# Kernel optimization log

Hardware: AMD Instinct MI355X
Metric: run time of the kernel (lower is better)

The kernel has to match this reference:

```python
import jax, jax.numpy as jnp
import numpy as np

DIM = 768
NUM_HEADS = 12
HEAD_DIM = DIM // NUM_HEADS
SCALE = HEAD_DIM ** -0.5


def setup_inputs() -> dict:
    key = jax.random.key(0)
    k1, k2, k3, k4 = jax.random.split(key, 4)
    B, N = 4, 2048
    x = jax.random.normal(k1, (B, N, DIM), dtype=jnp.float32)
    # torch Linear(dim, 3*dim, bias=False): weight [3*dim, dim]
    w_qkv = jax.random.normal(k2, (3 * DIM, DIM), dtype=jnp.float32) * (DIM ** -0.5)
    # proj: Linear(dim, dim) with bias
    w_proj = jax.random.normal(k3, (DIM, DIM), dtype=jnp.float32) * (DIM ** -0.5)
    b_proj = jax.random.normal(k4, (DIM,), dtype=jnp.float32) * 0.01
    return {"x": x, "w_qkv": w_qkv, "w_proj": w_proj, "b_proj": b_proj}


def reference(x, w_qkv, w_proj, b_proj):
    B, N, D = x.shape
    H, Hd = NUM_HEADS, HEAD_DIM
    qkv = x @ w_qkv.T                              # [B, N, 3D]
    qkv = qkv.reshape(B, N, 3, H, Hd)
    qkv = jnp.transpose(qkv, (2, 0, 3, 1, 4))      # [3, B, H, N, Hd]
    q, k, v = qkv[0], qkv[1], qkv[2]
    attn = jnp.einsum('bhnd,bhmd->bhnm', q, k) * SCALE  # [B, H, N, N]
    attn = jax.nn.softmax(attn, axis=-1)
    out = jnp.einsum('bhnm,bhmd->bhnd', attn, v)   # [B, H, N, Hd]
    out = jnp.transpose(out, (0, 2, 1, 3)).reshape(B, N, D)
    return out @ w_proj.T + b_proj
```

## Files before the change

kernel.cpp:

```cpp
#include <hip/hip_runtime.h>
#include <hip/hip_bf16.h>

#define DIM      768
#define NHEADS   12
#define HEADDIM  64
#define BATCH    4
#define SEQ      2048
#define NROWS    (BATCH * SEQ)
#define QKVCOLS  (3 * DIM)
#define SLOT     ((size_t)BATCH * NHEADS * SEQ * HEADDIM)

#define QSCALE_LOG2 0.18033688011112042f

typedef short bf16x8_t __attribute__((ext_vector_type(8)));
typedef short bf16x4_t __attribute__((ext_vector_type(4)));
typedef float f32x4_t  __attribute__((ext_vector_type(4)));

__device__ __forceinline__ short f2bf(float f) {
    union { __hip_bfloat16 h; short s; } u;
    u.h = __float2bfloat16(f);
    return u.s;
}

__device__ __forceinline__ float exp2_fast(float x) {
#if __has_builtin(__builtin_amdgcn_exp2f)
    return __builtin_amdgcn_exp2f(x);
#else
    return __expf(x * 0.6931471805599453f);
#endif
}

__device__ __forceinline__ void stage16(const __hip_bfloat16* g, __hip_bfloat16* l) {
    __builtin_amdgcn_global_load_lds(
        (const __attribute__((address_space(1))) void*)g,
        (__attribute__((address_space(3))) void*)l,
        16, 0, 0);
}

#define NX8  ((size_t)NROWS * DIM / 8)
#define NWQ8 ((size_t)QKVCOLS * DIM / 8)
#define NWP8 ((size_t)DIM * DIM / 8)

__global__ __launch_bounds__(256) void cvt_all(const float* __restrict__ X,
                                               const float* __restrict__ Wq,
                                               const float* __restrict__ Wp,
                                               __hip_bfloat16* __restrict__ Xb,
                                               __hip_bfloat16* __restrict__ Wqb,
                                               __hip_bfloat16* __restrict__ Wpb) {
    size_t i = (size_t)blockIdx.x * 256 + threadIdx.x;
    const float* src; __hip_bfloat16* dst; size_t off;
    if (i < NX8)                  { src = X;  dst = Xb;  off = i; }
    else if (i < NX8 + NWQ8)      { src = Wq; dst = Wqb; off = i - NX8; }
    else                          { src = Wp; dst = Wpb; off = i - NX8 - NWQ8; }
    float4 a = ((const float4*)src)[off * 2];
    float4 b = ((const float4*)src)[off * 2 + 1];
    bf16x8_t o;
    o[0] = f2bf(a.x); o[1] = f2bf(a.y); o[2] = f2bf(a.z); o[3] = f2bf(a.w);
    o[4] = f2bf(b.x); o[5] = f2bf(b.y); o[6] = f2bf(b.z); o[7] = f2bf(b.w);
    *(bf16x8_t*)(dst + off * 8) = o;
}

#define GEMM_CORE(Aptr, Bptr)                                                   \
    __shared__ __hip_bfloat16 As[128 * 64];                                     \
    __shared__ __hip_bfloat16 Bs[128 * 64];                                     \
    const int tid  = threadIdx.x;                                               \
    const int wave = tid >> 6;                                                  \
    const int lane = tid & 63;                                                  \
    const int quad = lane >> 4;                                                 \
    const int l16  = lane & 15;                                                 \
    const int wm   = wave >> 1;                                                 \
    const int wn   = wave & 1;                                                  \
    const int m0   = blockIdx.x * 128;                                          \
    const int n0   = blockIdx.y * 128;                                          \
    const int sr   = lane >> 3;                     \
    const int sc   = ((lane & 7) ^ sr) * 8;         \
    f32x4_t acc[4][4];                                                          \
    _Pragma("unroll")                                                           \
    for (int i = 0; i < 4; i++)                                                 \
        _Pragma("unroll")                                                       \
        for (int j = 0; j < 4; j++) acc[i][j] = (f32x4_t){0.f, 0.f, 0.f, 0.f};  \
    for (int k0 = 0; k0 < 768; k0 += 64) {                                      \
        __syncthreads();                                                        \
        _Pragma("unroll")                                                       \
        for (int i = 0; i < 4; i++) {                                           \
            int seg = wave * 4 + i;                                  \
            int row = seg * 8 + sr;                                             \
            stage16(Aptr + (size_t)(m0 + row) * 768 + k0 + sc, As + seg * 512); \
            stage16(Bptr + (size_t)(n0 + row) * 768 + k0 + sc, Bs + seg * 512); \
        }                                                                       \
        __syncthreads();               \
        _Pragma("unroll")                                                       \
        for (int kc = 0; kc < 2; kc++) {                                        \
            const int dsw = ((kc * 4 + quad) ^ (l16 & 7)) * 8;                  \
            bf16x8_t af[4], bfr[4];                                             \
            _Pragma("unroll")                                                   \
            for (int mt = 0; mt < 4; mt++)                                      \
                af[mt] = *(const bf16x8_t*)(As + (wm * 64 + mt * 16 + l16) * 64 + dsw); \
            _Pragma("unroll")                                                   \
            for (int nt = 0; nt < 4; nt++)                                      \
                bfr[nt] = *(const bf16x8_t*)(Bs + (wn * 64 + nt * 16 + l16) * 64 + dsw); \
            _Pragma("unroll")                                                   \
            for (int mt = 0; mt < 4; mt++)                                      \
                _Pragma("unroll")                                               \
                for (int nt = 0; nt < 4; nt++)                                  \
                    acc[mt][nt] = __builtin_amdgcn_mfma_f32_16x16x32_bf16(      \
                        af[mt], bfr[nt], acc[mt][nt], 0, 0, 0);                 \
        }                                                                       \
    }

__global__ __launch_bounds__(256) void qkv_gemm(const __hip_bfloat16* __restrict__ Xb,
                                                const __hip_bfloat16* __restrict__ Wqb,
                                                __hip_bfloat16* __restrict__ QKV) {
    GEMM_CORE(Xb, Wqb)

    const int bidx = m0 >> 11;
    const int seqb = (m0 & 2047) + wm * 64;
#pragma unroll
    for (int mt = 0; mt < 4; mt++) {
#pragma unroll
        for (int nt = 0; nt < 4; nt++) {
            int col   = n0 + wn * 64 + nt * 16 + l16;
            int which = col / 768;
            int rem   = col - which * 768;
            int h     = rem >> 6;
            int d     = rem & 63;
            if (which == 2) {
                size_t base = 2 * SLOT + (((size_t)bidx * NHEADS + h) * HEADDIM + d) * SEQ
                            + seqb + mt * 16 + quad * 4;
                bf16x4_t pk;
#pragma unroll
                for (int r = 0; r < 4; r++) pk[r] = f2bf(acc[mt][nt][r]);
                *(bf16x4_t*)(QKV + base) = pk;
            } else {
                float sc2 = (which == 0) ? QSCALE_LOG2 : 1.0f;
                size_t rowbase = ((size_t)bidx * NHEADS + h) * SEQ;
                size_t slotoff = (size_t)which * SLOT;
#pragma unroll
                for (int r = 0; r < 4; r++) {
                    int n = seqb + mt * 16 + quad * 4 + r;
                    QKV[slotoff + (rowbase + n) * HEADDIM + d] =
                        __float2bfloat16(acc[mt][nt][r] * sc2);
                }
            }
        }
    }
}

__global__ __launch_bounds__(512) void attn(const __hip_bfloat16* __restrict__ QKV,
                                            __hip_bfloat16* __restrict__ ATT) {
    __shared__ __hip_bfloat16 lds[384 * 72];
    __hip_bfloat16* Qs = lds;
    __hip_bfloat16* Ks = lds + 128 * 72;
    __hip_bfloat16* Vs = lds + 256 * 72;

    const int tid  = threadIdx.x;
    const int wave = tid >> 6;
    const int lane = tid & 63;
    const int quad = lane >> 4;
    const int l16  = lane & 15;
    const int qb   = blockIdx.x;
    const int bh   = blockIdx.y;
    const int b    = bh / NHEADS;
    const int h    = bh - b * NHEADS;

    const __hip_bfloat16* Qg = QKV + 0 * SLOT + (((size_t)b * NHEADS + h) * SEQ) * HEADDIM;
    const __hip_bfloat16* Kg = QKV + 1 * SLOT + (((size_t)b * NHEADS + h) * SEQ) * HEADDIM;
    const __hip_bfloat16* Vg = QKV + 2 * SLOT + (((size_t)b * NHEADS + h) * HEADDIM) * SEQ;

    const int rs = tid >> 3;
    const int es = (tid & 7) * 8;

#pragma unroll
    for (int i = 0; i < 2; i++) {
        int c = tid + i * 512;
        int r = c >> 3, e = (c & 7) * 8;
        *(bf16x8_t*)(Qs + r * 72 + e) =
            *(const bf16x8_t*)(Qg + (size_t)(qb * 128 + r) * HEADDIM + e);
    }
    *(bf16x8_t*)(Ks + rs * 72 + es) = *(const bf16x8_t*)(Kg + (size_t)rs * HEADDIM + es);
    *(bf16x8_t*)(Vs + rs * 72 + es) = *(const bf16x8_t*)(Vg + (size_t)rs * SEQ + es);
    __syncthreads();

    bf16x8_t aq[2];
#pragma unroll
    for (int kc = 0; kc < 2; kc++)
        aq[kc] = *(const bf16x8_t*)(Qs + (wave * 16 + l16) * 72 + kc * 32 + quad * 8);

    __hip_bfloat16* Pw = Qs + wave * 16 * 72;

    f32x4_t o[4];
#pragma unroll
    for (int dt = 0; dt < 4; dt++) o[dt] = (f32x4_t){0.f, 0.f, 0.f, 0.f};
    float l_i[4] = {0.f, 0.f, 0.f, 0.f};

    for (int t = 0; t < SEQ / 64; t++) {
        const int cur = t & 1;
        __hip_bfloat16* Kc = Ks + cur * 64 * 72;
        __hip_bfloat16* Vc = Vs + cur * 64 * 72;

        bf16x8_t nk, nv;
        const bool has_next = (t + 1 < SEQ / 64);
        if (has_next) {
            int n0 = (t + 1) * 64;
            nk = *(const bf16x8_t*)(Kg + (size_t)(n0 + rs) * HEADDIM + es);
            nv = *(const bf16x8_t*)(Vg + (size_t)rs * SEQ + n0 + es);
        }

        f32x4_t s[4];
#pragma unroll
        for (int nt = 0; nt < 4; nt++) {
            s[nt] = (f32x4_t){0.f, 0.f, 0.f, 0.f};
#pragma unroll
            for (int kc = 0; kc < 2; kc++) {
                bf16x8_t bk = *(const bf16x8_t*)(Kc + (nt * 16 + l16) * 72 + kc * 32 + quad * 8);
                s[nt] = __builtin_amdgcn_mfma_f32_16x16x32_bf16(aq[kc], bk, s[nt], 0, 0, 0);
            }
        }

#pragma unroll
        for (int nt = 0; nt < 4; nt++)
#pragma unroll
            for (int r = 0; r < 4; r++) {
                float p = exp2_fast(s[nt][r]);
                s[nt][r] = p;
                l_i[r] += p;
            }

#pragma unroll
        for (int nt = 0; nt < 4; nt++)
#pragma unroll
            for (int r = 0; r < 4; r++)
                Pw[(quad * 4 + r) * 72 + nt * 16 + l16] = __float2bfloat16(s[nt][r]);

#pragma unroll
        for (int kc = 0; kc < 2; kc++) {
            bf16x8_t ap = *(const bf16x8_t*)(Pw + l16 * 72 + kc * 32 + quad * 8);
#pragma unroll
            for (int dt = 0; dt < 4; dt++) {
                bf16x8_t bv = *(const bf16x8_t*)(Vc + (dt * 16 + l16) * 72 + kc * 32 + quad * 8);
                o[dt] = __builtin_amdgcn_mfma_f32_16x16x32_bf16(ap, bv, o[dt], 0, 0, 0);
            }
        }

        if (has_next) {
            __hip_bfloat16* Kn = Ks + (1 - cur) * 64 * 72;
            __hip_bfloat16* Vn = Vs + (1 - cur) * 64 * 72;
            *(bf16x8_t*)(Kn + rs * 72 + es) = nk;
            *(bf16x8_t*)(Vn + rs * 72 + es) = nv;
        }
        __syncthreads();
    }

#pragma unroll
    for (int msk = 1; msk < 16; msk <<= 1)
#pragma unroll
        for (int r = 0; r < 4; r++) l_i[r] += __shfl_xor(l_i[r], msk, 16);

#pragma unroll
    for (int dt = 0; dt < 4; dt++) {
#pragma unroll
        for (int r = 0; r < 4; r++) {
            int n = qb * 128 + wave * 16 + quad * 4 + r;
            int d = dt * 16 + l16;
            float val = o[dt][r] / l_i[r];
            ATT[((size_t)b * SEQ + n) * DIM + h * HEADDIM + d] = __float2bfloat16(val);
        }
    }
}

__global__ __launch_bounds__(256) void proj_gemm(const __hip_bfloat16* __restrict__ A,
                                                 const __hip_bfloat16* __restrict__ B,
                                                 const float* __restrict__ bias,
                                                 float* __restrict__ OUT) {
    GEMM_CORE(A, B)

#pragma unroll
    for (int mt = 0; mt < 4; mt++) {
#pragma unroll
        for (int nt = 0; nt < 4; nt++) {
            int col = n0 + wn * 64 + nt * 16 + l16;
            float bv = bias[col];
#pragma unroll
            for (int r = 0; r < 4; r++) {
                int row = m0 + wm * 64 + mt * 16 + quad * 4 + r;
                OUT[(size_t)row * 768 + col] = acc[mt][nt][r] + bv;
            }
        }
    }
}

extern "C" void kernel_launch(void* const* d_in, const int* in_sizes, int n_in,
                              void* d_out, int out_size, void* d_ws, size_t ws_size,
                              hipStream_t stream) {
    const float* x      = (const float*)d_in[0];
    const float* w_qkv  = (const float*)d_in[1];
    const float* w_proj = (const float*)d_in[2];
    const float* b_proj = (const float*)d_in[3];
    float* out = (float*)d_out;

    __hip_bfloat16* qkv_ws = (__hip_bfloat16*)d_ws;
    __hip_bfloat16* xb     = qkv_ws + 3 * SLOT;
    __hip_bfloat16* att_ws = xb;
    __hip_bfloat16* wqb    = xb + (size_t)NROWS * DIM;
    __hip_bfloat16* wpb    = wqb + (size_t)QKVCOLS * DIM;

    int cvt_blocks = (int)((NX8 + NWQ8 + NWP8) / 256);
    cvt_all<<<cvt_blocks, 256, 0, stream>>>(x, w_qkv, w_proj, xb, wqb, wpb);

    dim3 g1(NROWS / 128, QKVCOLS / 128);
    qkv_gemm<<<g1, 256, 0, stream>>>(xb, wqb, qkv_ws);

    dim3 g2(SEQ / 128, BATCH * NHEADS);
    attn<<<g2, 512, 0, stream>>>(qkv_ws, att_ws);

    dim3 g3(NROWS / 128, DIM / 128);
    proj_gemm<<<g3, 256, 0, stream>>>(att_ws, wpb, b_proj, out);
}
```

Before: 236.3 us.

## Compute transposed S tile so P stays in registers and feeds PV MFMA directly

The attention loop now computes S^T (K as the A operand), so each lane holds P values in the layout the 16x16x16 bf16 MFMA expects as its B operand, removing the per-tile LDS write/read round trip for P. Q is loaded once into registers, then its LDS region is reused for the K/V double buffers, shrinking shared memory, and launch bounds request more blocks per CU. The QKV GEMM swaps operands so its epilogue writes Q/K as packed 4-element vectors and V with strided scalar stores, and the output is written as packed bf16x4. The tradeoff is twice as many smaller MFMAs for PV, and the now-scalar strided V stores.

Result: no change. 237.7 us (+0.6%).

```diff
diff --git a/kernel.cpp b/kernel.cpp
--- a/kernel.cpp
+++ b/kernel.cpp
@@ -108,50 +108,44 @@
         }                                                                       \
     }
 
-__global__ __launch_bounds__(256) void qkv_gemm(const __hip_bfloat16* __restrict__ Xb,
-                                                const __hip_bfloat16* __restrict__ Wqb,
+__global__ __launch_bounds__(256) void qkv_gemm(const __hip_bfloat16* __restrict__ Wqb,
+                                                const __hip_bfloat16* __restrict__ Xb,
                                                 __hip_bfloat16* __restrict__ QKV) {
-    GEMM_CORE(Xb, Wqb)
-
-    const int bidx = m0 >> 11;
-    const int seqb = (m0 & 2047) + wm * 64;
+    GEMM_CORE(Wqb, Xb)
+
+    const int bidx = n0 >> 11;
+    const int nb   = (n0 & 2047) + wn * 64;
 #pragma unroll
     for (int mt = 0; mt < 4; mt++) {
+        int colbase = m0 + wm * 64 + mt * 16;
+        int which   = colbase / 768;
+        int rem     = colbase - which * 768;
+        int h       = rem >> 6;
+        int dbase   = (rem & 63) + quad * 4;
 #pragma unroll
         for (int nt = 0; nt < 4; nt++) {
-            int col   = n0 + wn * 64 + nt * 16 + l16;
-            int which = col / 768;
-            int rem   = col - which * 768;
-            int h     = rem >> 6;
-            int d     = rem & 63;
+            int n = nb + nt * 16 + l16;
             if (which == 2) {
-                size_t base = 2 * SLOT + (((size_t)bidx * NHEADS + h) * HEADDIM + d) * SEQ
-                            + seqb + mt * 16 + quad * 4;
-                bf16x4_t pk;
-#pragma unroll
-                for (int r = 0; r < 4; r++) pk[r] = f2bf(acc[mt][nt][r]);
-                *(bf16x4_t*)(QKV + base) = pk;
+                size_t base = 2 * SLOT + (((size_t)bidx * NHEADS + h) * HEADDIM + dbase) * SEQ + n;
+#pragma unroll
+                for (int r = 0; r < 4; r++)
+                    QKV[base + (size_t)r * SEQ] = __float2bfloat16(acc[mt][nt][r]);
             } else {
                 float sc2 = (which == 0) ? QSCALE_LOG2 : 1.0f;
-                size_t rowbase = ((size_t)bidx * NHEADS + h) * SEQ;
-                size_t slotoff = (size_t)which * SLOT;
-#pragma unroll
-                for (int r = 0; r < 4; r++) {
-                    int n = seqb + mt * 16 + quad * 4 + r;
-                    QKV[slotoff + (rowbase + n) * HEADDIM + d] =
-                        __float2bfloat16(acc[mt][nt][r] * sc2);
-                }
-            }
-        }
-    }
-}
-
-__global__ __launch_bounds__(512) void attn(const __hip_bfloat16* __restrict__ QKV,
-                                            __hip_bfloat16* __restrict__ ATT) {
-    __shared__ __hip_bfloat16 lds[384 * 72];
-    __hip_bfloat16* Qs = lds;
-    __hip_bfloat16* Ks = lds + 128 * 72;
-    __hip_bfloat16* Vs = lds + 256 * 72;
+                size_t addr = (size_t)which * SLOT
+                            + (((size_t)bidx * NHEADS + h) * SEQ + n) * HEADDIM + dbase;
+                bf16x4_t pk;
+#pragma unroll
+                for (int r = 0; r < 4; r++) pk[r] = f2bf(acc[mt][nt][r] * sc2);
+                *(bf16x4_t*)(QKV + addr) = pk;
+            }
+        }
+    }
+}
+
+__global__ __launch_bounds__(512, 6) void attn(const __hip_bfloat16* __restrict__ QKV,
+                                               __hip_bfloat16* __restrict__ ATT) {
+    __shared__ __hip_bfloat16 lds[288 * 64];
 
     const int tid  = threadIdx.x;
     const int wave = tid >> 6;
@@ -174,97 +168,91 @@
     for (int i = 0; i < 2; i++) {
         int c = tid + i * 512;
         int r = c >> 3, e = (c & 7) * 8;
-        *(bf16x8_t*)(Qs + r * 72 + e) =
+        *(bf16x8_t*)(lds + r * 72 + e) =
             *(const bf16x8_t*)(Qg + (size_t)(qb * 128 + r) * HEADDIM + e);
     }
-    *(bf16x8_t*)(Ks + rs * 72 + es) = *(const bf16x8_t*)(Kg + (size_t)rs * HEADDIM + es);
-    *(bf16x8_t*)(Vs + rs * 72 + es) = *(const bf16x8_t*)(Vg + (size_t)rs * SEQ + es);
+    *(bf16x8_t*)(lds + 9216 + rs * 72 + es)  = *(const bf16x8_t*)(Kg + (size_t)rs * HEADDIM + es);
+    *(bf16x8_t*)(lds + 13824 + rs * 72 + es) = *(const bf16x8_t*)(Vg + (size_t)rs * SEQ + es);
     __syncthreads();
 
     bf16x8_t aq[2];
 #pragma unroll
     for (int kc = 0; kc < 2; kc++)
-        aq[kc] = *(const bf16x8_t*)(Qs + (wave * 16 + l16) * 72 + kc * 32 + quad * 8);
-
-    __hip_bfloat16* Pw = Qs + wave * 16 * 72;
+        aq[kc] = *(const bf16x8_t*)(lds + (wave * 16 + l16) * 72 + kc * 32 + quad * 8);
+    __syncthreads();
 
     f32x4_t o[4];
 #pragma unroll
     for (int dt = 0; dt < 4; dt++) o[dt] = (f32x4_t){0.f, 0.f, 0.f, 0.f};
-    float l_i[4] = {0.f, 0.f, 0.f, 0.f};
+    float l_part = 0.f;
 
     for (int t = 0; t < SEQ / 64; t++) {
-        const int cur = t & 1;
-        __hip_bfloat16* Kc = Ks + cur * 64 * 72;
-        __hip_bfloat16* Vc = Vs + cur * 64 * 72;
+        const int cur  = t & 1;
+        const int boff = cur ? 0 : 9216;
+        const __hip_bfloat16* Kc = lds + boff;
+        const __hip_bfloat16* Vc = lds + boff + 4608;
 
         bf16x8_t nk, nv;
         const bool has_next = (t + 1 < SEQ / 64);
         if (has_next) {
-            int n0 = (t + 1) * 64;
-            nk = *(const bf16x8_t*)(Kg + (size_t)(n0 + rs) * HEADDIM + es);
-            nv = *(const bf16x8_t*)(Vg + (size_t)rs * SEQ + n0 + es);
+            int nn0 = (t + 1) * 64;
+            nk = *(const bf16x8_t*)(Kg + (size_t)(nn0 + rs) * HEADDIM + es);
+            nv = *(const bf16x8_t*)(Vg + (size_t)rs * SEQ + nn0 + es);
         }
 
         f32x4_t s[4];
 #pragma unroll
-        for (int nt = 0; nt < 4; nt++) {
-            s[nt] = (f32x4_t){0.f, 0.f, 0.f, 0.f};
-#pragma unroll
-            for (int kc = 0; kc < 2; kc++) {
-                bf16x8_t bk = *(const bf16x8_t*)(Kc + (nt * 16 + l16) * 72 + kc * 32 + quad * 8);
-                s[nt] = __builtin_amdgcn_mfma_f32_16x16x32_bf16(aq[kc], bk, s[nt], 0, 0, 0);
-            }
-        }
-
-#pragma unroll
-        for (int nt = 0; nt < 4; nt++)
+        for (int mt = 0; mt < 4; mt++) s[mt] = (f32x4_t){0.f, 0.f, 0.f, 0.f};
+#pragma unroll
+        for (int kc = 0; kc < 2; kc++) {
+#pragma unroll
+            for (int mt = 0; mt < 4; mt++) {
+                bf16x8_t bk = *(const bf16x8_t*)(Kc + (mt * 16 + l16) * 72 + kc * 32 + quad * 8);
+                s[mt] = __builtin_amdgcn_mfma_f32_16x16x32_bf16(bk, aq[kc], s[mt], 0, 0, 0);
+            }
+        }
+
+#pragma unroll
+        for (int mt = 0; mt < 4; mt++)
 #pragma unroll
             for (int r = 0; r < 4; r++) {
-                float p = exp2_fast(s[nt][r]);
-                s[nt][r] = p;
-                l_i[r] += p;
-            }
-
-#pragma unroll
-        for (int nt = 0; nt < 4; nt++)
-#pragma unroll
-            for (int r = 0; r < 4; r++)
-                Pw[(quad * 4 + r) * 72 + nt * 16 + l16] = __float2bfloat16(s[nt][r]);
-
-#pragma unroll
-        for (int kc = 0; kc < 2; kc++) {
-            bf16x8_t ap = *(const bf16x8_t*)(Pw + l16 * 72 + kc * 32 + quad * 8);
+                float p = exp2_fast(s[mt][r]);
+                s[mt][r] = p;
+                l_part += p;
+            }
+
+#pragma unroll
+        for (int kb = 0; kb < 4; kb++) {
+            bf16x4_t pb;
+#pragma unroll
+            for (int j = 0; j < 4; j++) pb[j] = f2bf(s[kb][j]);
 #pragma unroll
             for (int dt = 0; dt < 4; dt++) {
-                bf16x8_t bv = *(const bf16x8_t*)(Vc + (dt * 16 + l16) * 72 + kc * 32 + quad * 8);
-                o[dt] = __builtin_amdgcn_mfma_f32_16x16x32_bf16(ap, bv, o[dt], 0, 0, 0);
+                bf16x4_t av = *(const bf16x4_t*)(Vc + (dt * 16 + l16) * 72 + kb * 16 + quad * 4);
+                o[dt] = __builtin_amdgcn_mfma_f32_16x16x16bf16_1k(av, pb, o[dt], 0, 0, 0);
             }
         }
 
         if (has_next) {
-            __hip_bfloat16* Kn = Ks + (1 - cur) * 64 * 72;
-            __hip_bfloat16* Vn = Vs + (1 - cur) * 64 * 72;
-            *(bf16x8_t*)(Kn + rs * 72 + es) = nk;
-            *(bf16x8_t*)(Vn + rs * 72 + es) = nv;
+            const int aoff = cur ? 9216 : 0;
+            *(bf16x8_t*)(lds + aoff + rs * 72 + es)        = nk;
+            *(bf16x8_t*)(lds + aoff + 4608 + rs * 72 + es) = nv;
         }
         __syncthreads();
     }
 
-#pragma unroll
-    for (int msk = 1; msk < 16; msk <<= 1)
-#pragma unroll
-        for (int r = 0; r < 4; r++) l_i[r] += __shfl_xor(l_i[r], msk, 16);
-
+    l_part += __shfl_xor(l_part, 16);
+    l_part += __shfl_xor(l_part, 32);
+    float inv = 1.f / l_part;
+
+    const int n = qb * 128 + wave * 16 + l16;
+    __hip_bfloat16* orow = ATT + ((size_t)b * SEQ + n) * DIM + h * HEADDIM + quad * 4;
 #pragma unroll
     for (int dt = 0; dt < 4; dt++) {
-#pragma unroll
-        for (int r = 0; r < 4; r++) {
-            int n = qb * 128 + wave * 16 + quad * 4 + r;
-            int d = dt * 16 + l16;
-            float val = o[dt][r] / l_i[r];
-            ATT[((size_t)b * SEQ + n) * DIM + h * HEADDIM + d] = __float2bfloat16(val);
-        }
+        bf16x4_t pk;
+#pragma unroll
+        for (int r = 0; r < 4; r++) pk[r] = f2bf(o[dt][r] * inv);
+        *(bf16x4_t*)(orow + dt * 16) = pk;
     }
 }
 
@@ -307,8 +295,8 @@
     int cvt_blocks = (int)((NX8 + NWQ8 + NWP8) / 256);
     cvt_all<<<cvt_blocks, 256, 0, stream>>>(x, w_qkv, w_proj, xb, wqb, wpb);
 
-    dim3 g1(NROWS / 128, QKVCOLS / 128);
-    qkv_gemm<<<g1, 256, 0, stream>>>(xb, wqb, qkv_ws);
+    dim3 g1(QKVCOLS / 128, NROWS / 128);
+    qkv_gemm<<<g1, 256, 0, stream>>>(wqb, xb, qkv_ws);
 
     dim3 g2(SEQ / 128, BATCH * NHEADS);
     attn<<<g2, 512, 0, stream>>>(qkv_ws, att_ws);
```
